# Kernel tuning notes

Measured on AMD Instinct MI355X. Metric: run time of the kernel, lower is better.

Reference implementation:

```python
import jax, jax.numpy as jnp
import numpy as np

# Dimensions: B jets, P max particles, C coords, F features, K neighbors,
# H hidden units, O MLP output dim. Edge feature dim E = 2*(C+F).
B, P, C, F, K, H, O = 256, 128, 2, 7, 16, 128, 256
E = 2 * (C + F)
BIG = 1e9  # distance assigned to invalid (padded) neighbors


def setup_inputs() -> dict:
    key = jax.random.key(0)
    k1, k2, k3, k4 = jax.random.split(key, 4)
    raw = jax.random.normal(k1, (B, P, C + F), dtype=jnp.float32)
    # per-jet particle counts in [K+2, P]; padding is contiguous at the end
    lengths = jax.random.randint(k2, (B,), K + 2, P + 1)
    mask = (jnp.arange(P)[None, :] < lengths[:, None]).astype(jnp.float32)  # [B,P]
    # zero out padded rows and append mask as the last column (as the layer expects)
    x = jnp.concatenate([raw * mask[..., None], mask[..., None]], axis=-1)  # [B,P,C+F+1]
    W1 = jax.random.normal(k3, (E, H), dtype=jnp.float32) * (1.0 / np.sqrt(E))
    b1 = jnp.zeros((H,), dtype=jnp.float32)
    W2 = jax.random.normal(k4, (H, O), dtype=jnp.float32) * (1.0 / np.sqrt(H))
    b2 = jnp.zeros((O,), dtype=jnp.float32)
    return {"x": x, "W1": W1, "b1": b1, "W2": W2, "b2": b2}


def reference(x, W1, b1, W2, b2):
    coords = x[..., :C]          # [B,P,C]
    feats = x[..., C:-1]         # [B,P,F]
    mask = x[..., -1]            # [B,P] 1=real particle, 0=padding
    valid = mask > 0

    # --- kNN on coordinates (masked, vectorized over jets) ---
    diff = coords[:, :, None, :] - coords[:, None, :, :]      # [B,P,P,C]
    # squared distance: same ordering as tf.norm, avoids sqrt-at-zero issues
    dist2 = jnp.sum(diff * diff, axis=-1)                      # [B,P,P]
    dist2 = jnp.where(valid[:, None, :], dist2, BIG)           # mask padded neighbors
    _, idx = jax.lax.top_k(-dist2, K + 1)                      # [B,P,K+1]
    idx = idx[..., 1:]                                         # drop self -> [B,P,K]

    # --- gather neighbor coords/features ---
    idx_flat = idx.reshape(B, P * K)
    nbr_c = jnp.take_along_axis(coords, idx_flat[..., None], axis=1).reshape(B, P, K, C)
    nbr_f = jnp.take_along_axis(feats, idx_flat[..., None], axis=1).reshape(B, P, K, F)
    ctr_c = jnp.broadcast_to(coords[:, :, None, :], (B, P, K, C))
    ctr_f = jnp.broadcast_to(feats[:, :, None, :], (B, P, K, F))

    # edge features: [coord_i, feat_i, coord_j - coord_i, feat_j - feat_i]
    edge = jnp.concatenate([ctr_c, ctr_f, nbr_c - ctr_c, nbr_f - ctr_f], axis=-1)  # [B,P,K,E]

    # --- MLP + mean aggregation over neighbors ---
    h = jax.nn.relu(edge @ W1 + b1)   # [B,P,K,H]
    h = jax.nn.relu(h @ W2 + b2)      # [B,P,K,O]
    avg = jnp.mean(h, axis=2)         # [B,P,O]

    # append mask column; zero out padded particles (matches _fix_number_of_particles)
    out = jnp.concatenate([avg, jnp.ones((B, P, 1), avg.dtype)], axis=-1) * mask[..., None]
    return out
```

## Files before the change

### kernel.cpp

```cpp
#include <hip/hip_runtime.h>

#define BB 256
#define PP 128
#define KK 16
#define HH 128
#define OO 256
#define EE 18
#define XCH 10
#define BIGD 1000000000.0f
#define GPT 4
#define XS 11

typedef __bf16 bf16x8 __attribute__((ext_vector_type(8)));
typedef __bf16 bf16x4 __attribute__((ext_vector_type(4)));
typedef float  f32x4  __attribute__((ext_vector_type(4)));

__global__ __launch_bounds__(256) void pack_w_kernel(const float* __restrict__ W1,
                                                     const float* __restrict__ W2,
                                                     __bf16* __restrict__ W2p,
                                                     __bf16* __restrict__ W1p) {
    const int t = blockIdx.x * 256 + threadIdx.x;
    if (t < 32768) {
        const int j  = t & 7;
        const int l  = (t >> 3) & 63;
        const int ks = (t >> 9) & 3;
        const int ct = t >> 11;
        const int row = ks * 32 + ((l >> 4) * 8) + j;
        const int col = ct * 16 + (l & 15);
        W2p[t] = (__bf16)W2[row * OO + col];
    } else {
        const int t2 = t - 32768;
        const int j  = t2 & 7;
        const int l  = (t2 >> 3) & 63;
        const int nt = t2 >> 9;
        const int k  = ((l >> 4) * 8) + j;
        const int n  = nt * 16 + (l & 15);
        W1p[t2] = (k < EE) ? (__bf16)W1[k * HH + n] : (__bf16)0.0f;
    }
}

__global__ __launch_bounds__(256, 4) void mlp_kernel(const float* __restrict__ x,
                                                     const __bf16* __restrict__ W1p,
                                                     const float* __restrict__ b1,
                                                     const __bf16* __restrict__ W2p,
                                                     const float* __restrict__ b2,
                                                     float* __restrict__ out) {
    __shared__ float  sxr[PP * XS];
    __shared__ __bf16 sh1A[16 * 64 * 8];
    __shared__ int    sknn[GPT][KK];

    const int tid = threadIdx.x;
    const int lane = tid & 63;
    const int w = tid >> 6;
    const int quad = lane >> 4;
    const int lcol = lane & 15;

    const int pbase = blockIdx.x * GPT;
    const int bidx = pbase >> 7;
    const int i0 = pbase & (PP - 1);
    const float* xb = x + (size_t)bidx * PP * XCH;
    float* outrow = out + (size_t)pbase * (OO + 1);

    const float m0 = xb[(i0 + 0) * XCH + 9];
    const float m1 = xb[(i0 + 1) * XCH + 9];
    const float m2 = xb[(i0 + 2) * XCH + 9];
    const float m3 = xb[(i0 + 3) * XCH + 9];
    if (m0 == 0.0f && m1 == 0.0f && m2 == 0.0f && m3 == 0.0f) {
        for (int o = tid; o < GPT * (OO + 1); o += 256) outrow[o] = 0.0f;
        return;
    }

    for (int t = tid; t < PP * XCH; t += 256) {
        const int r = t / XCH;
        const int c = t - r * XCH;
        sxr[r * XS + c] = xb[t];
    }
    __syncthreads();

    const int i = i0 + w;
    const float mw = (w == 0) ? m0 : (w == 1) ? m1 : (w == 2) ? m2 : m3;

    if (mw != 0.0f) {
        const float cix = sxr[i * XS + 0];
        const float ciy = sxr[i * XS + 1];

        const int j0 = lane, j1 = lane + 64;
        float d0, d1;
        {
            const float mj = sxr[j0 * XS + 9];
            const float dx = cix - sxr[j0 * XS + 0];
            const float dy = ciy - sxr[j0 * XS + 1];
            d0 = __fadd_rn(__fmul_rn(dx, dx), __fmul_rn(dy, dy));
            if (mj <= 0.0f || j0 == i) d0 = BIGD;
        }
        {
            const float mj = sxr[j1 * XS + 9];
            const float dx = cix - sxr[j1 * XS + 0];
            const float dy = ciy - sxr[j1 * XS + 1];
            d1 = __fadd_rn(__fmul_rn(dx, dx), __fmul_rn(dy, dy));
            if (mj <= 0.0f || j1 == i) d1 = BIGD;
        }

        const unsigned d0b = __float_as_uint(d0);
        const unsigned d1b = __float_as_uint(d1);

        unsigned long long A0 = ~0ull, A1 = ~0ull, W0 = 0ull, W1 = 0ull;
        int need = KK;

        auto step = [&](unsigned long long q0, unsigned long long q1) {
            const unsigned long long z0 = A0 & q0;
            const unsigned long long z1 = A1 & q1;
            const int c = __popcll(z0) + __popcll(z1);
            if (c == need) { W0 |= z0; W1 |= z1; A0 = A1 = 0ull; need = 0; }
            else if (c > need) { A0 = z0; A1 = z1; }
            else { W0 |= z0; W1 |= z1; need -= c; A0 &= ~z0; A1 &= ~z1; }
        };

#pragma unroll 1
        for (int bp = 30; bp >= 0; --bp) {
            if (need == 0) break;
            const unsigned long long q0 = __ballot(((d0b >> bp) & 1u) == 0u);
            const unsigned long long q1 = __ballot(((d1b >> bp) & 1u) == 0u);
            step(q0, q1);
        }
        if (need) step(~0ull, 0ull);
        {
            const unsigned long long M5 = 0x00000000FFFFFFFFull;
            const unsigned long long M4 = 0x0000FFFF0000FFFFull;
            const unsigned long long M3 = 0x00FF00FF00FF00FFull;
            const unsigned long long M2 = 0x0F0F0F0F0F0F0F0Full;
            const unsigned long long M1 = 0x3333333333333333ull;
            const unsigned long long M0 = 0x5555555555555555ull;
            if (need) step(M5, M5);
            if (need) step(M4, M4);
            if (need) step(M3, M3);
            if (need) step(M2, M2);
            if (need) step(M1, M1);
            if (need) step(M0, M0);
        }
        W0 |= A0; W1 |= A1;

        unsigned int mb0 = __builtin_amdgcn_mbcnt_lo((unsigned)(W0 & 0xffffffffull), 0u);
        mb0 = __builtin_amdgcn_mbcnt_hi((unsigned)(W0 >> 32), mb0);
        unsigned int mb1 = __builtin_amdgcn_mbcnt_lo((unsigned)(W1 & 0xffffffffull), 0u);
        mb1 = __builtin_amdgcn_mbcnt_hi((unsigned)(W1 >> 32), mb1);
        const int base1 = __popcll(W0);

        if ((W0 >> lane) & 1ull) sknn[w][mb0] = j0;
        if ((W1 >> lane) & 1ull) sknn[w][base1 + mb1] = j1;
    } else {
        if (lane < KK) sknn[w][lane] = 0;
    }

    const int jn = sknn[w][lcol];
    bf16x8 ef;
#pragma unroll
    for (int e = 0; e < 8; ++e) {
        const int c = quad * 8 + e;
        const int cA = (c < 9) ? c : ((c < 18) ? c - 9 : 0);
        const int cN = (c >= 9 && c < 18) ? c - 9 : 0;
        const float rA = sxr[i * XS + cA];
        const float rN = sxr[jn * XS + cN];
        float vv = (c < 9) ? rA : (rN - rA);
        if (c >= 18) vv = 0.0f;
        ef[e] = (__bf16)vv;
    }

    bf16x8 wf[8];
#pragma unroll
    for (int nt = 0; nt < 8; ++nt)
        wf[nt] = *(const bf16x8*)&W1p[(size_t)((nt * 64 + lane) * 8)];

    const f32x4 z4 = {0.0f, 0.0f, 0.0f, 0.0f};
    f32x4 h[8];
#pragma unroll
    for (int nt = 0; nt < 8; ++nt)
        h[nt] = __builtin_amdgcn_mfma_f32_16x16x32_bf16(wf[nt], ef, z4, 0, 0, 0);

#pragma unroll
    for (int nt = 0; nt < 8; ++nt) {
        const f32x4 bv = *(const f32x4*)&b1[nt * 16 + quad * 4];
        const int ks = nt >> 1;
        const int lp = (((nt * 2 + (quad >> 1)) & 3) << 4) | lcol;
        bf16x4 hv;
#pragma unroll
        for (int r = 0; r < 4; ++r)
            hv[r] = (__bf16)fmaxf(h[nt][r] + bv[r], 0.0f);
        *(bf16x4*)&sh1A[((ks * GPT + w) * 64 + lp) * 8 + (quad & 1) * 4] = hv;
    }
    __syncthreads();

    f32x4 acc[GPT][4];
#pragma unroll
    for (int g = 0; g < GPT; ++g)
#pragma unroll
        for (int ct = 0; ct < 4; ++ct) acc[g][ct] = z4;

#pragma unroll
    for (int ks = 0; ks < 4; ++ks) {
        bf16x8 af[GPT], bfr[4];
#pragma unroll
        for (int g = 0; g < GPT; ++g)
            af[g] = *(const bf16x8*)&sh1A[((ks * GPT + g) * 64 + lane) * 8];
#pragma unroll
        for (int ct = 0; ct < 4; ++ct)
            bfr[ct] = *(const bf16x8*)&W2p[(size_t)((((w * 4 + ct) * 4 + ks) * 64 + lane) * 8)];
#pragma unroll
        for (int g = 0; g < GPT; ++g)
#pragma unroll
            for (int ct = 0; ct < 4; ++ct)
                acc[g][ct] = __builtin_amdgcn_mfma_f32_16x16x32_bf16(
                    af[g], bfr[ct], acc[g][ct], 0, 0, 0);
    }

    float val[4];
#pragma unroll
    for (int g = 0; g < GPT; ++g) {
#pragma unroll
        for (int ct = 0; ct < 4; ++ct) {
            const int col = w * 64 + ct * 16 + lcol;
            const float bc = b2[col];
            float s = 0.0f;
#pragma unroll
            for (int r = 0; r < 4; ++r) s += fmaxf(acc[g][ct][r] + bc, 0.0f);
            s += __shfl_xor(s, 16, 64);
            s += __shfl_xor(s, 32, 64);
            if (quad == g) val[ct] = s;
        }
    }
    const float mq = (quad == 0) ? m0 : (quad == 1) ? m1 : (quad == 2) ? m2 : m3;
    const float msc = mq * (1.0f / KK);
#pragma unroll
    for (int ct = 0; ct < 4; ++ct)
        outrow[(size_t)quad * (OO + 1) + w * 64 + ct * 16 + lcol] = val[ct] * msc;
    if (tid < GPT) {
        const float mt = (tid == 0) ? m0 : (tid == 1) ? m1 : (tid == 2) ? m2 : m3;
        outrow[(size_t)tid * (OO + 1) + OO] = mt;
    }
}

extern "C" void kernel_launch(void* const* d_in, const int* in_sizes, int n_in,
                              void* d_out, int out_size, void* d_ws, size_t ws_size,
                              hipStream_t stream) {
    const float* x  = (const float*)d_in[0];
    const float* W1 = (const float*)d_in[1];
    const float* b1 = (const float*)d_in[2];
    const float* W2 = (const float*)d_in[3];
    const float* b2 = (const float*)d_in[4];
    float* out = (float*)d_out;

    __bf16* W2p = (__bf16*)d_ws;
    __bf16* W1p = (__bf16*)((char*)d_ws + 65536);

    pack_w_kernel<<<144, 256, 0, stream>>>(W1, W2, W2p, W1p);

    const int nblocks = (BB * PP) / GPT;
    mlp_kernel<<<nblocks, 256, 0, stream>>>(x, W1p, b1, W2p, b2, out);
}
```

Baseline: 134.7 us.

## Process eight particles per block with double-buffered GEMM1/GEMM2 overlap

Each block now handles two groups of four particles. W2 fragments and b2 are loaded into registers once per block, and the jet's x tile is staged in shared memory once per block. The second group's kNN selection and first GEMM are issued while the first group's second-GEMM MFMAs are in flight, using a double-buffered shared hidden tile. In exchange, register pressure rises, and launch bounds drop to two blocks per CU, which may reduce occupancy and latency hiding.

```diff
diff --git a/kernel.cpp b/kernel.cpp
--- a/kernel.cpp
+++ b/kernel.cpp
@@ -8,7 +8,7 @@
 #define EE 18
 #define XCH 10
 #define BIGD 1000000000.0f
-#define GPT 4
+#define NPB 8
 #define XS 11
 
 typedef __bf16 bf16x8 __attribute__((ext_vector_type(8)));
@@ -39,15 +39,15 @@
     }
 }
 
-__global__ __launch_bounds__(256, 4) void mlp_kernel(const float* __restrict__ x,
+__global__ __launch_bounds__(256, 2) void mlp_kernel(const float* __restrict__ x,
                                                      const __bf16* __restrict__ W1p,
                                                      const float* __restrict__ b1,
                                                      const __bf16* __restrict__ W2p,
                                                      const float* __restrict__ b2,
                                                      float* __restrict__ out) {
     __shared__ float  sxr[PP * XS];
-    __shared__ __bf16 sh1A[16 * 64 * 8];
-    __shared__ int    sknn[GPT][KK];
+    __shared__ __bf16 sh1A[2][16 * 64 * 8];
+    __shared__ int    sknn[4][KK];
 
     const int tid = threadIdx.x;
     const int lane = tid & 63;
@@ -55,18 +55,27 @@
     const int quad = lane >> 4;
     const int lcol = lane & 15;
 
-    const int pbase = blockIdx.x * GPT;
+    const int pbase = blockIdx.x * NPB;
     const int bidx = pbase >> 7;
     const int i0 = pbase & (PP - 1);
     const float* xb = x + (size_t)bidx * PP * XCH;
     float* outrow = out + (size_t)pbase * (OO + 1);
 
-    const float m0 = xb[(i0 + 0) * XCH + 9];
-    const float m1 = xb[(i0 + 1) * XCH + 9];
-    const float m2 = xb[(i0 + 2) * XCH + 9];
-    const float m3 = xb[(i0 + 3) * XCH + 9];
-    if (m0 == 0.0f && m1 == 0.0f && m2 == 0.0f && m3 == 0.0f) {
-        for (int o = tid; o < GPT * (OO + 1); o += 256) outrow[o] = 0.0f;
+    bf16x8 bfr[4][4];
+#pragma unroll
+    for (int ks = 0; ks < 4; ++ks)
+#pragma unroll
+        for (int ct = 0; ct < 4; ++ct)
+            bfr[ks][ct] = *(const bf16x8*)&W2p[(size_t)((((w * 4 + ct) * 4 + ks) * 64 + lane) * 8)];
+    float bc[4];
+#pragma unroll
+    for (int ct = 0; ct < 4; ++ct) bc[ct] = b2[w * 64 + ct * 16 + lcol];
+
+    bool anylive = false;
+#pragma unroll
+    for (int g = 0; g < NPB; ++g) anylive |= (xb[(i0 + g) * XCH + 9] != 0.0f);
+    if (!anylive) {
+        for (int o = tid; o < NPB * (OO + 1); o += 256) outrow[o] = 0.0f;
         return;
     }
 
@@ -77,166 +86,175 @@
     }
     __syncthreads();
 
-    const int i = i0 + w;
-    const float mw = (w == 0) ? m0 : (w == 1) ? m1 : (w == 2) ? m2 : m3;
-
-    if (mw != 0.0f) {
-        const float cix = sxr[i * XS + 0];
-        const float ciy = sxr[i * XS + 1];
-
-        const int j0 = lane, j1 = lane + 64;
-        float d0, d1;
-        {
-            const float mj = sxr[j0 * XS + 9];
-            const float dx = cix - sxr[j0 * XS + 0];
-            const float dy = ciy - sxr[j0 * XS + 1];
-            d0 = __fadd_rn(__fmul_rn(dx, dx), __fmul_rn(dy, dy));
-            if (mj <= 0.0f || j0 == i) d0 = BIGD;
-        }
-        {
-            const float mj = sxr[j1 * XS + 9];
-            const float dx = cix - sxr[j1 * XS + 0];
-            const float dy = ciy - sxr[j1 * XS + 1];
-            d1 = __fadd_rn(__fmul_rn(dx, dx), __fmul_rn(dy, dy));
-            if (mj <= 0.0f || j1 == i) d1 = BIGD;
-        }
-
-        const unsigned d0b = __float_as_uint(d0);
-        const unsigned d1b = __float_as_uint(d1);
-
-        unsigned long long A0 = ~0ull, A1 = ~0ull, W0 = 0ull, W1 = 0ull;
-        int need = KK;
-
-        auto step = [&](unsigned long long q0, unsigned long long q1) {
-            const unsigned long long z0 = A0 & q0;
-            const unsigned long long z1 = A1 & q1;
-            const int c = __popcll(z0) + __popcll(z1);
-            if (c == need) { W0 |= z0; W1 |= z1; A0 = A1 = 0ull; need = 0; }
-            else if (c > need) { A0 = z0; A1 = z1; }
-            else { W0 |= z0; W1 |= z1; need -= c; A0 &= ~z0; A1 &= ~z1; }
-        };
-
+    auto knn_select = [&](int ip) {
+        if (sxr[ip * XS + 9] != 0.0f) {
+            const float cix = sxr[ip * XS + 0];
+            const float ciy = sxr[ip * XS + 1];
+            const int j0 = lane, j1 = lane + 64;
+            float d0, d1;
+            {
+                const float mj = sxr[j0 * XS + 9];
+                const float dx = cix - sxr[j0 * XS + 0];
+                const float dy = ciy - sxr[j0 * XS + 1];
+                d0 = __fadd_rn(__fmul_rn(dx, dx), __fmul_rn(dy, dy));
+                if (mj <= 0.0f || j0 == ip) d0 = BIGD;
+            }
+            {
+                const float mj = sxr[j1 * XS + 9];
+                const float dx = cix - sxr[j1 * XS + 0];
+                const float dy = ciy - sxr[j1 * XS + 1];
+                d1 = __fadd_rn(__fmul_rn(dx, dx), __fmul_rn(dy, dy));
+                if (mj <= 0.0f || j1 == ip) d1 = BIGD;
+            }
+            const unsigned d0b = __float_as_uint(d0);
+            const unsigned d1b = __float_as_uint(d1);
+
+            unsigned long long A0 = ~0ull, A1 = ~0ull, W0 = 0ull, W1 = 0ull;
+            int need = KK;
+            auto step = [&](unsigned long long q0, unsigned long long q1) {
+                const unsigned long long z0 = A0 & q0;
+                const unsigned long long z1 = A1 & q1;
+                const int c = __popcll(z0) + __popcll(z1);
+                if (c == need) { W0 |= z0; W1 |= z1; A0 = A1 = 0ull; need = 0; }
+                else if (c > need) { A0 = z0; A1 = z1; }
+                else { W0 |= z0; W1 |= z1; need -= c; A0 &= ~z0; A1 &= ~z1; }
+            };
 #pragma unroll 1
-        for (int bp = 30; bp >= 0; --bp) {
-            if (need == 0) break;
-            const unsigned long long q0 = __ballot(((d0b >> bp) & 1u) == 0u);
-            const unsigned long long q1 = __ballot(((d1b >> bp) & 1u) == 0u);
-            step(q0, q1);
-        }
-        if (need) step(~0ull, 0ull);
-        {
-            const unsigned long long M5 = 0x00000000FFFFFFFFull;
-            const unsigned long long M4 = 0x0000FFFF0000FFFFull;
-            const unsigned long long M3 = 0x00FF00FF00FF00FFull;
-            const unsigned long long M2 = 0x0F0F0F0F0F0F0F0Full;
-            const unsigned long long M1 = 0x3333333333333333ull;
-            const unsigned long long M0 = 0x5555555555555555ull;
-            if (need) step(M5, M5);
-            if (need) step(M4, M4);
-            if (need) step(M3, M3);
-            if (need) step(M2, M2);
-            if (need) step(M1, M1);
-            if (need) step(M0, M0);
-        }
-        W0 |= A0; W1 |= A1;
-
-        unsigned int mb0 = __builtin_amdgcn_mbcnt_lo((unsigned)(W0 & 0xffffffffull), 0u);
-        mb0 = __builtin_amdgcn_mbcnt_hi((unsigned)(W0 >> 32), mb0);
-        unsigned int mb1 = __builtin_amdgcn_mbcnt_lo((unsigned)(W1 & 0xffffffffull), 0u);
-        mb1 = __builtin_amdgcn_mbcnt_hi((unsigned)(W1 >> 32), mb1);
-        const int base1 = __popcll(W0);
-
-        if ((W0 >> lane) & 1ull) sknn[w][mb0] = j0;
-        if ((W1 >> lane) & 1ull) sknn[w][base1 + mb1] = j1;
-    } else {
-        if (lane < KK) sknn[w][lane] = 0;
-    }
-
-    const int jn = sknn[w][lcol];
-    bf16x8 ef;
-#pragma unroll
-    for (int e = 0; e < 8; ++e) {
-        const int c = quad * 8 + e;
-        const int cA = (c < 9) ? c : ((c < 18) ? c - 9 : 0);
-        const int cN = (c >= 9 && c < 18) ? c - 9 : 0;
-        const float rA = sxr[i * XS + cA];
-        const float rN = sxr[jn * XS + cN];
-        float vv = (c < 9) ? rA : (rN - rA);
-        if (c >= 18) vv = 0.0f;
-        ef[e] = (__bf16)vv;
-    }
-
-    bf16x8 wf[8];
-#pragma unroll
-    for (int nt = 0; nt < 8; ++nt)
-        wf[nt] = *(const bf16x8*)&W1p[(size_t)((nt * 64 + lane) * 8)];
+            for (int bp = 30; bp >= 0; --bp) {
+                if (need == 0) break;
+                const unsigned long long q0 = __ballot(((d0b >> bp) & 1u) == 0u);
+                const unsigned long long q1 = __ballot(((d1b >> bp) & 1u) == 0u);
+                step(q0, q1);
+            }
+            if (need) step(~0ull, 0ull);
+            {
+                const unsigned long long M5 = 0x00000000FFFFFFFFull;
+                const unsigned long long M4 = 0x0000FFFF0000FFFFull;
+                const unsigned long long M3 = 0x00FF00FF00FF00FFull;
+                const unsigned long long M2 = 0x0F0F0F0F0F0F0F0Full;
+                const unsigned long long M1 = 0x3333333333333333ull;
+                const unsigned long long M0 = 0x5555555555555555ull;
+                if (need) step(M5, M5);
+                if (need) step(M4, M4);
+                if (need) step(M3, M3);
+                if (need) step(M2, M2);
+                if (need) step(M1, M1);
+                if (need) step(M0, M0);
+            }
+            W0 |= A0; W1 |= A1;
+
+            unsigned int mb0 = __builtin_amdgcn_mbcnt_lo((unsigned)(W0 & 0xffffffffull), 0u);
+            mb0 = __builtin_amdgcn_mbcnt_hi((unsigned)(W0 >> 32), mb0);
+            unsigned int mb1 = __builtin_amdgcn_mbcnt_lo((unsigned)(W1 & 0xffffffffull), 0u);
+            mb1 = __builtin_amdgcn_mbcnt_hi((unsigned)(W1 >> 32), mb1);
+            const int base1 = __popcll(W0);
+            if ((W0 >> lane) & 1ull) sknn[w][mb0] = j0;
+            if ((W1 >> lane) & 1ull) sknn[w][base1 + mb1] = j1;
+        } else {
+            if (lane < KK) sknn[w][lane] = 0;
+        }
+    };
+
+    auto build_ef = [&](int ip) -> bf16x8 {
+        const int jn = sknn[w][lcol];
+        bf16x8 ef;
+#pragma unroll
+        for (int e = 0; e < 8; ++e) {
+            const int c = quad * 8 + e;
+            const int cA = (c < 9) ? c : ((c < 18) ? c - 9 : 0);
+            const int cN = (c >= 9 && c < 18) ? c - 9 : 0;
+            const float rA = sxr[ip * XS + cA];
+            const float rN = sxr[jn * XS + cN];
+            float vv = (c < 9) ? rA : (rN - rA);
+            if (c >= 18) vv = 0.0f;
+            ef[e] = (__bf16)vv;
+        }
+        return ef;
+    };
 
     const f32x4 z4 = {0.0f, 0.0f, 0.0f, 0.0f};
-    f32x4 h[8];
-#pragma unroll
-    for (int nt = 0; nt < 8; ++nt)
-        h[nt] = __builtin_amdgcn_mfma_f32_16x16x32_bf16(wf[nt], ef, z4, 0, 0, 0);
-
-#pragma unroll
-    for (int nt = 0; nt < 8; ++nt) {
-        const f32x4 bv = *(const f32x4*)&b1[nt * 16 + quad * 4];
-        const int ks = nt >> 1;
-        const int lp = (((nt * 2 + (quad >> 1)) & 3) << 4) | lcol;
-        bf16x4 hv;
-#pragma unroll
-        for (int r = 0; r < 4; ++r)
-            hv[r] = (__bf16)fmaxf(h[nt][r] + bv[r], 0.0f);
-        *(bf16x4*)&sh1A[((ks * GPT + w) * 64 + lp) * 8 + (quad & 1) * 4] = hv;
-    }
+
+    auto gemm1_to = [&](int sbuf, bf16x8 ef) {
+        bf16x8 wf[8];
+#pragma unroll
+        for (int nt = 0; nt < 8; ++nt)
+            wf[nt] = *(const bf16x8*)&W1p[(size_t)((nt * 64 + lane) * 8)];
+        f32x4 h[8];
+#pragma unroll
+        for (int nt = 0; nt < 8; ++nt)
+            h[nt] = __builtin_amdgcn_mfma_f32_16x16x32_bf16(wf[nt], ef, z4, 0, 0, 0);
+#pragma unroll
+        for (int nt = 0; nt < 8; ++nt) {
+            const f32x4 bv = *(const f32x4*)&b1[nt * 16 + quad * 4];
+            const int ks = nt >> 1;
+            const int lp = (((nt * 2 + (quad >> 1)) & 3) << 4) | lcol;
+            bf16x4 hv;
+#pragma unroll
+            for (int r = 0; r < 4; ++r)
+                hv[r] = (__bf16)fmaxf(h[nt][r] + bv[r], 0.0f);
+            *(bf16x4*)&sh1A[sbuf][((ks * 4 + w) * 64 + lp) * 8 + (quad & 1) * 4] = hv;
+        }
+    };
+
+    auto gemm2_issue = [&](int sbuf, f32x4 (&acc)[4][4]) {
+#pragma unroll
+        for (int g = 0; g < 4; ++g)
+#pragma unroll
+            for (int ct = 0; ct < 4; ++ct) acc[g][ct] = z4;
+#pragma unroll
+        for (int ks = 0; ks < 4; ++ks) {
+            bf16x8 af[4];
+#pragma unroll
+            for (int g = 0; g < 4; ++g)
+                af[g] = *(const bf16x8*)&sh1A[sbuf][((ks * 4 + g) * 64 + lane) * 8];
+#pragma unroll
+            for (int g = 0; g < 4; ++g)
+#pragma unroll
+                for (int ct = 0; ct < 4; ++ct)
+                    acc[g][ct] = __builtin_amdgcn_mfma_f32_16x16x32_bf16(
+                        af[g], bfr[ks][ct], acc[g][ct], 0, 0, 0);
+        }
+    };
+
+    auto epi2_store = [&](f32x4 (&acc)[4][4], int gb) {
+        float val[4];
+#pragma unroll
+        for (int g = 0; g < 4; ++g) {
+#pragma unroll
+            for (int ct = 0; ct < 4; ++ct) {
+                float s = 0.0f;
+#pragma unroll
+                for (int r = 0; r < 4; ++r) s += fmaxf(acc[g][ct][r] + bc[ct], 0.0f);
+                s += __shfl_xor(s, 16, 64);
+                s += __shfl_xor(s, 32, 64);
+                if (quad == g) val[ct] = s;
+            }
+        }
+        const float msc = sxr[(i0 + gb + quad) * XS + 9] * (1.0f / KK);
+#pragma unroll
+        for (int ct = 0; ct < 4; ++ct)
+            outrow[(size_t)(gb + quad) * (OO + 1) + w * 64 + ct * 16 + lcol] = val[ct] * msc;
+    };
+
+    const int ip0 = i0 + w;
+    const int ip1 = i0 + 4 + w;
+
+    knn_select(ip0);
+    gemm1_to(0, build_ef(ip0));
     __syncthreads();
 
-    f32x4 acc[GPT][4];
-#pragma unroll
-    for (int g = 0; g < GPT; ++g)
-#pragma unroll
-        for (int ct = 0; ct < 4; ++ct) acc[g][ct] = z4;
-
-#pragma unroll
-    for (int ks = 0; ks < 4; ++ks) {
-        bf16x8 af[GPT], bfr[4];
-#pragma unroll
-        for (int g = 0; g < GPT; ++g)
-            af[g] = *(const bf16x8*)&sh1A[((ks * GPT + g) * 64 + lane) * 8];
-#pragma unroll
-        for (int ct = 0; ct < 4; ++ct)
-            bfr[ct] = *(const bf16x8*)&W2p[(size_t)((((w * 4 + ct) * 4 + ks) * 64 + lane) * 8)];
-#pragma unroll
-        for (int g = 0; g < GPT; ++g)
-#pragma unroll
-            for (int ct = 0; ct < 4; ++ct)
-                acc[g][ct] = __builtin_amdgcn_mfma_f32_16x16x32_bf16(
-                    af[g], bfr[ct], acc[g][ct], 0, 0, 0);
-    }
-
-    float val[4];
-#pragma unroll
-    for (int g = 0; g < GPT; ++g) {
-#pragma unroll
-        for (int ct = 0; ct < 4; ++ct) {
-            const int col = w * 64 + ct * 16 + lcol;
-            const float bc = b2[col];
-            float s = 0.0f;
-#pragma unroll
-            for (int r = 0; r < 4; ++r) s += fmaxf(acc[g][ct][r] + bc, 0.0f);
-            s += __shfl_xor(s, 16, 64);
-            s += __shfl_xor(s, 32, 64);
-            if (quad == g) val[ct] = s;
-        }
-    }
-    const float mq = (quad == 0) ? m0 : (quad == 1) ? m1 : (quad == 2) ? m2 : m3;
-    const float msc = mq * (1.0f / KK);
-#pragma unroll
-    for (int ct = 0; ct < 4; ++ct)
-        outrow[(size_t)quad * (OO + 1) + w * 64 + ct * 16 + lcol] = val[ct] * msc;
-    if (tid < GPT) {
-        const float mt = (tid == 0) ? m0 : (tid == 1) ? m1 : (tid == 2) ? m2 : m3;
-        outrow[(size_t)tid * (OO + 1) + OO] = mt;
-    }
+    f32x4 acc0[4][4];
+    gemm2_issue(0, acc0);
+    knn_select(ip1);
+    gemm1_to(1, build_ef(ip1));
+    epi2_store(acc0, 0);
+    __syncthreads();
+
+    f32x4 acc1[4][4];
+    gemm2_issue(1, acc1);
+    epi2_store(acc1, 4);
+
+    if (tid < NPB) outrow[(size_t)tid * (OO + 1) + OO] = sxr[(i0 + tid) * XS + 9];
 }
 
 extern "C" void kernel_launch(void* const* d_in, const int* in_sizes, int n_in,
@@ -254,6 +272,6 @@
 
     pack_w_kernel<<<144, 256, 0, stream>>>(W1, W2, W2p, W1p);
 
-    const int nblocks = (BB * PP) / GPT;
+    const int nblocks = (BB * PP) / NPB;
     mlp_kernel<<<nblocks, 256, 0, stream>>>(x, W1p, b1, W2p, b2, out);
 }
```

After: 156.6 us. 1.16x slower.
